# Performance work log

Hardware: AMD Instinct MI355X
Metric: run time of the kernel (lower is better)

## Reference

```python
import jax, jax.numpy as jnp
import numpy as np

INPUT_SIZE = 784
HIDDEN_SIZE = 256
NUM_CLASSES = 10
BATCH = 32768


def setup_inputs() -> dict:
    key = jax.random.key(0)
    k_x, k_w1, k_b1, k_w2, k_b2 = jax.random.split(key, 5)
    return {
        "x": jax.random.normal(k_x, (BATCH, INPUT_SIZE), dtype=jnp.float32),
        "fc1_weight": jax.random.normal(k_w1, (HIDDEN_SIZE, INPUT_SIZE), dtype=jnp.float32),
        "fc1_bias": jax.random.normal(k_b1, (HIDDEN_SIZE,), dtype=jnp.float32),
        "fc2_weight": jax.random.normal(k_w2, (NUM_CLASSES, HIDDEN_SIZE), dtype=jnp.float32),
        "fc2_bias": jax.random.normal(k_b2, (NUM_CLASSES,), dtype=jnp.float32),
    }


def reference(x, fc1_weight, fc1_bias, fc2_weight, fc2_bias):
    # hidden = x @ W1^T + b1, ReLU
    hidden = jnp.einsum("bi,hi->bh", x, fc1_weight) + fc1_bias
    activated = jnp.maximum(hidden, 0.0)
    # output = activated @ W2^T + b2
    logits = jnp.einsum("bh,ch->bc", activated, fc2_weight) + fc2_bias
    return jax.nn.softmax(logits, axis=-1)
```

## Files before the change

### kernel.cpp

```cpp
#include <hip/hip_runtime.h>
#include <math.h>

#define BATCH_N   32768
#define IN_F      784
#define HID_F     256
#define NCLS      10
#define BM        64
#define BK        32
#define NKT       25
#define NTHREADS  256

typedef __attribute__((ext_vector_type(8))) short short8;
typedef __attribute__((ext_vector_type(4))) float f32x4;

#define WS_W1H 0
#define WS_W1L 409600

union S8U { short8 s; uint4 u; };

__device__ __forceinline__ void cvt8(float4 a, float4 b, short8* hi, short8* lo) {
    const unsigned M = 0xFFFF0000u;
    const unsigned ux = __float_as_uint(a.x), uy = __float_as_uint(a.y),
                   uz = __float_as_uint(a.z), uw = __float_as_uint(a.w),
                   vx = __float_as_uint(b.x), vy = __float_as_uint(b.y),
                   vz = __float_as_uint(b.z), vw = __float_as_uint(b.w);
    S8U h, l;
    h.u.x = (ux >> 16) | (uy & M);
    h.u.y = (uz >> 16) | (uw & M);
    h.u.z = (vx >> 16) | (vy & M);
    h.u.w = (vz >> 16) | (vw & M);
    const float rx = a.x - __uint_as_float(ux & M);
    const float ry = a.y - __uint_as_float(uy & M);
    const float rz = a.z - __uint_as_float(uz & M);
    const float rw = a.w - __uint_as_float(uw & M);
    const float sx = b.x - __uint_as_float(vx & M);
    const float sy = b.y - __uint_as_float(vy & M);
    const float sz = b.z - __uint_as_float(vz & M);
    const float sw_ = b.w - __uint_as_float(vw & M);
    l.u.x = (__float_as_uint(rx) >> 16) | (__float_as_uint(ry) & M);
    l.u.y = (__float_as_uint(rz) >> 16) | (__float_as_uint(rw) & M);
    l.u.z = (__float_as_uint(sx) >> 16) | (__float_as_uint(sy) & M);
    l.u.w = (__float_as_uint(sz) >> 16) | (__float_as_uint(sw_) & M);
    *hi = h.s; *lo = l.s;
}

__global__ __launch_bounds__(256)
void prep_w1_kernel(const float* __restrict__ w1, char* __restrict__ ws) {
    const int s    = blockIdx.x * 256 + threadIdx.x;
    const int lane = s & 63, ct = (s >> 6) & 15, kt = s >> 10;
    const int n    = ct * 16 + (lane & 15);
    const int k0   = kt * 32 + (lane >> 4) * 8;
    float4 a = make_float4(0.f, 0.f, 0.f, 0.f), b = a;
    if (k0 + 7 < IN_F) {
        const float* p = w1 + (size_t)n * IN_F + k0;
        a = *(const float4*)p;
        b = *(const float4*)(p + 4);
    }
    short8 hi, lo;
    cvt8(a, b, &hi, &lo);
    *(short8*)(ws + WS_W1H + (size_t)s * 16) = hi;
    *(short8*)(ws + WS_W1L + (size_t)s * 16) = lo;
}

__global__ __launch_bounds__(NTHREADS, 2)
void mlp_mfma_kernel(const float* __restrict__ x,
                     const char*  __restrict__ wsb,
                     const float* __restrict__ b1,
                     const float* __restrict__ w2,
                     const float* __restrict__ b2,
                     float* __restrict__ out)
{
    __shared__ float hid[BM * HID_F];

    const int tid  = threadIdx.x;
    const int wv   = tid >> 6;
    const int lane = tid & 63;
    const int m    = lane & 15;
    const int quad = lane >> 4;
    const int row0 = blockIdx.x * BM;
    const int kq   = quad * 8;

    f32x4 acc[4][4];
    #pragma unroll
    for (int a = 0; a < 4; ++a)
        #pragma unroll
        for (int b = 0; b < 4; ++b)
            acc[a][b] = (f32x4){0.f, 0.f, 0.f, 0.f};

    const float* xb[4];
    #pragma unroll
    for (int rt = 0; rt < 4; ++rt)
        xb[rt] = x + (size_t)(row0 + rt * 16 + m) * IN_F;

    const char* bhp = wsb + WS_W1H + ((size_t)(wv * 4) * 64 + lane) * 16;
    const char* blp = wsb + WS_W1L + ((size_t)(wv * 4) * 64 + lane) * 16;

    float4 xc[4][2];
    short8 bhc[4], blc[4];
    #pragma unroll
    for (int rt = 0; rt < 4; ++rt) {
        xc[rt][0] = *(const float4*)(xb[rt] + kq);
        xc[rt][1] = *(const float4*)(xb[rt] + kq + 4);
    }
    #pragma unroll
    for (int c = 0; c < 4; ++c) {
        bhc[c] = *(const short8*)(bhp + c * 1024);
        blc[c] = *(const short8*)(blp + c * 1024);
    }

    #pragma unroll 8
    for (int kt = 0; kt < NKT - 1; ++kt) {
        short8 bhn[4], bln[4];
        #pragma unroll
        for (int c = 0; c < 4; ++c) {
            bhn[c] = *(const short8*)(bhp + (size_t)(kt + 1) * 16384 + c * 1024);
            bln[c] = *(const short8*)(blp + (size_t)(kt + 1) * 16384 + c * 1024);
        }
        int kon = (kt + 1) * BK + kq;
        kon = kon > (IN_F - 8) ? (IN_F - 8) : kon;
        float4 xn[4][2];
        #pragma unroll
        for (int rt = 0; rt < 4; ++rt) {
            xn[rt][0] = *(const float4*)(xb[rt] + kon);
            xn[rt][1] = *(const float4*)(xb[rt] + kon + 4);
        }
        short8 ah[4], al[4];
        #pragma unroll
        for (int rt = 0; rt < 4; ++rt)
            cvt8(xc[rt][0], xc[rt][1], &ah[rt], &al[rt]);
        #pragma unroll
        for (int rt = 0; rt < 4; ++rt)
            #pragma unroll
            for (int c = 0; c < 4; ++c) {
                acc[rt][c] = __builtin_amdgcn_mfma_f32_16x16x32_bf16(ah[rt], bhc[c], acc[rt][c], 0, 0, 0);
                acc[rt][c] = __builtin_amdgcn_mfma_f32_16x16x32_bf16(al[rt], bhc[c], acc[rt][c], 0, 0, 0);
                acc[rt][c] = __builtin_amdgcn_mfma_f32_16x16x32_bf16(ah[rt], blc[c], acc[rt][c], 0, 0, 0);
            }
        #pragma unroll
        for (int rt = 0; rt < 4; ++rt) {
            xc[rt][0] = xn[rt][0];
            xc[rt][1] = xn[rt][1];
        }
        #pragma unroll
        for (int c = 0; c < 4; ++c) { bhc[c] = bhn[c]; blc[c] = bln[c]; }
    }

    {
        short8 ah[4], al[4];
        #pragma unroll
        for (int rt = 0; rt < 4; ++rt)
            cvt8(xc[rt][0], xc[rt][1], &ah[rt], &al[rt]);
        if (quad >= 2) {
            const short8 zz = {0, 0, 0, 0, 0, 0, 0, 0};
            #pragma unroll
            for (int rt = 0; rt < 4; ++rt) { ah[rt] = zz; al[rt] = zz; }
        }
        #pragma unroll
        for (int rt = 0; rt < 4; ++rt)
            #pragma unroll
            for (int c = 0; c < 4; ++c) {
                acc[rt][c] = __builtin_amdgcn_mfma_f32_16x16x32_bf16(ah[rt], bhc[c], acc[rt][c], 0, 0, 0);
                acc[rt][c] = __builtin_amdgcn_mfma_f32_16x16x32_bf16(al[rt], bhc[c], acc[rt][c], 0, 0, 0);
                acc[rt][c] = __builtin_amdgcn_mfma_f32_16x16x32_bf16(ah[rt], blc[c], acc[rt][c], 0, 0, 0);
            }
    }

    #pragma unroll
    for (int c = 0; c < 4; ++c) {
        const int col = (wv * 4 + c) * 16 + m;
        const float bv = b1[col];
        #pragma unroll
        for (int rt = 0; rt < 4; ++rt)
            #pragma unroll
            for (int reg = 0; reg < 4; ++reg) {
                const int row = rt * 16 + quad * 4 + reg;
                hid[row * 256 + (col ^ ((row & 7) << 2))] = fmaxf(acc[rt][c][reg] + bv, 0.f);
            }
    }
    __syncthreads();

    const int rl = wv * 16 + m;
    const int sw = (rl & 7) << 2;
    const float* hrow = hid + rl * 256;
    float lg[NCLS];
    #pragma unroll
    for (int c = 0; c < NCLS; ++c) lg[c] = 0.f;
    #pragma unroll
    for (int i = 0; i < 8; ++i) {
        const int h0 = i * 32 + quad * 8;
        const float4 h1 = *(const float4*)(hrow + (h0 ^ sw));
        const float4 h2 = *(const float4*)(hrow + ((h0 + 4) ^ sw));
        #pragma unroll
        for (int c = 0; c < NCLS; ++c) {
            const float4 wa = *(const float4*)(w2 + c * HID_F + h0);
            const float4 wb = *(const float4*)(w2 + c * HID_F + h0 + 4);
            lg[c] += h1.x * wa.x + h1.y * wa.y + h1.z * wa.z + h1.w * wa.w
                   + h2.x * wb.x + h2.y * wb.y + h2.z * wb.z + h2.w * wb.w;
        }
    }
    #pragma unroll
    for (int c = 0; c < NCLS; ++c) {
        float v = lg[c];
        v += __shfl_xor(v, 16);
        v += __shfl_xor(v, 32);
        lg[c] = v;
    }
    if (quad == 0) {
        float mx = -1e30f;
        #pragma unroll
        for (int c = 0; c < NCLS; ++c) { lg[c] += b2[c]; mx = fmaxf(mx, lg[c]); }
        float s = 0.f;
        #pragma unroll
        for (int c = 0; c < NCLS; ++c) { lg[c] = __expf(lg[c] - mx); s += lg[c]; }
        const float inv = 1.f / s;
        float* o = out + (size_t)(row0 + rl) * NCLS;
        #pragma unroll
        for (int c = 0; c < NCLS; ++c) o[c] = lg[c] * inv;
    }
}

extern "C" void kernel_launch(void* const* d_in, const int* in_sizes, int n_in,
                              void* d_out, int out_size, void* d_ws, size_t ws_size,
                              hipStream_t stream)
{
    const float* x  = (const float*)d_in[0];
    const float* w1 = (const float*)d_in[1];
    const float* b1 = (const float*)d_in[2];
    const float* w2 = (const float*)d_in[3];
    const float* b2 = (const float*)d_in[4];
    float* out = (float*)d_out;

    hipLaunchKernelGGL(prep_w1_kernel, dim3(100), dim3(256), 0, stream,
                       w1, (char*)d_ws);
    hipLaunchKernelGGL(mlp_mfma_kernel, dim3(BATCH_N / BM), dim3(NTHREADS), 0, stream,
                       x, (const char*)d_ws, b1, w2, b2, out);
}
```

Baseline: 200.6 us.

## Stage split-bf16 X tiles in LDS with 512-thread blocks and double buffering

The GEMM1 mainloop now loads each X row segment once per block, converts it to bf16 hi/lo and stores it in double-buffered, XOR-swizzled LDS. Eight waves split the work as 2 row groups by 4 column groups, replacing per-wave redundant global X loads and repeated conversions. The hidden tile is written to shared memory in two halves to shrink LDS, and the epilogue is reworked so 8 threads per row each reduce a slice. In exchange the loop gains a __syncthreads per 64-wide k step, and the W1 fragments are no longer register-prefetched a step ahead.

```diff
diff --git a/kernel.cpp b/kernel.cpp
--- a/kernel.cpp
+++ b/kernel.cpp
@@ -6,9 +6,8 @@
 #define HID_F     256
 #define NCLS      10
 #define BM        64
-#define BK        32
-#define NKT       25
-#define NTHREADS  256
+#define NTHREADS  512
+#define NRND      13
 
 typedef __attribute__((ext_vector_type(8))) short short8;
 typedef __attribute__((ext_vector_type(4))) float f32x4;
@@ -62,7 +61,7 @@
     *(short8*)(ws + WS_W1L + (size_t)s * 16) = lo;
 }
 
-__global__ __launch_bounds__(NTHREADS, 2)
+__global__ __launch_bounds__(NTHREADS, 4)
 void mlp_mfma_kernel(const float* __restrict__ x,
                      const char*  __restrict__ wsb,
                      const float* __restrict__ b1,
@@ -70,153 +69,174 @@
                      const float* __restrict__ b2,
                      float* __restrict__ out)
 {
-    __shared__ float hid[BM * HID_F];
+    __shared__ short8 xh[2][512];
+    __shared__ short8 xl[2][512];
+    __shared__ float  hid[64 * 128];
 
     const int tid  = threadIdx.x;
+    const int lane = tid & 63;
     const int wv   = tid >> 6;
-    const int lane = tid & 63;
+    const int wc   = wv & 3;
+    const int wr   = wv >> 2;
     const int m    = lane & 15;
     const int quad = lane >> 4;
     const int row0 = blockIdx.x * BM;
-    const int kq   = quad * 8;
-
-    f32x4 acc[4][4];
-    #pragma unroll
-    for (int a = 0; a < 4; ++a)
+
+    const int slr = tid >> 3;
+    const int sks = tid & 7;
+    const float* xs = x + (size_t)(row0 + slr) * IN_F + sks * 8;
+    const int swidx = slr * 8 + (sks ^ (slr & 7));
+
+    const int rb  = (wr * 32 + m) * 8;
+    const int sl0 = rb + (quad ^ (m & 7));
+    const int sl1 = rb + ((4 + quad) ^ (m & 7));
+
+    const char* bhp = wsb + WS_W1H + ((size_t)(wc * 4) * 64 + lane) * 16;
+    const char* blp = wsb + WS_W1L + ((size_t)(wc * 4) * 64 + lane) * 16;
+
+    f32x4 acc[2][4];
+    #pragma unroll
+    for (int a = 0; a < 2; ++a)
         #pragma unroll
         for (int b = 0; b < 4; ++b)
             acc[a][b] = (f32x4){0.f, 0.f, 0.f, 0.f};
 
-    const float* xb[4];
-    #pragma unroll
-    for (int rt = 0; rt < 4; ++rt)
-        xb[rt] = x + (size_t)(row0 + rt * 16 + m) * IN_F;
-
-    const char* bhp = wsb + WS_W1H + ((size_t)(wv * 4) * 64 + lane) * 16;
-    const char* blp = wsb + WS_W1L + ((size_t)(wv * 4) * 64 + lane) * 16;
-
-    float4 xc[4][2];
-    short8 bhc[4], blc[4];
-    #pragma unroll
-    for (int rt = 0; rt < 4; ++rt) {
-        xc[rt][0] = *(const float4*)(xb[rt] + kq);
-        xc[rt][1] = *(const float4*)(xb[rt] + kq + 4);
-    }
-    #pragma unroll
-    for (int c = 0; c < 4; ++c) {
-        bhc[c] = *(const short8*)(bhp + c * 1024);
-        blc[c] = *(const short8*)(blp + c * 1024);
-    }
-
-    #pragma unroll 8
-    for (int kt = 0; kt < NKT - 1; ++kt) {
-        short8 bhn[4], bln[4];
+    {
+        float4 a = *(const float4*)(xs);
+        float4 b = *(const float4*)(xs + 4);
+        short8 hi, lo;
+        cvt8(a, b, &hi, &lo);
+        xh[0][swidx] = hi;
+        xl[0][swidx] = lo;
+    }
+    __syncthreads();
+
+    int cur = 0;
+    for (int r = 0; r < NRND - 1; ++r) {
+        const int kn = (r + 1) * 64 + sks * 8;
+        float4 xa = make_float4(0.f, 0.f, 0.f, 0.f), xb = xa;
+        if (kn + 7 < IN_F) {
+            xa = *(const float4*)(xs + (r + 1) * 64);
+            xb = *(const float4*)(xs + (r + 1) * 64 + 4);
+        }
+        #pragma unroll
+        for (int kk = 0; kk < 2; ++kk) {
+            const int kt = r * 2 + kk;
+            short8 bh[4], bl[4];
+            #pragma unroll
+            for (int c = 0; c < 4; ++c) {
+                bh[c] = *(const short8*)(bhp + (size_t)kt * 16384 + c * 1024);
+                bl[c] = *(const short8*)(blp + (size_t)kt * 16384 + c * 1024);
+            }
+            const int sl = kk ? sl1 : sl0;
+            short8 ah[2], al[2];
+            #pragma unroll
+            for (int rt = 0; rt < 2; ++rt) {
+                ah[rt] = xh[cur][sl + rt * 128];
+                al[rt] = xl[cur][sl + rt * 128];
+            }
+            #pragma unroll
+            for (int rt = 0; rt < 2; ++rt)
+                #pragma unroll
+                for (int c = 0; c < 4; ++c) {
+                    acc[rt][c] = __builtin_amdgcn_mfma_f32_16x16x32_bf16(ah[rt], bh[c], acc[rt][c], 0, 0, 0);
+                    acc[rt][c] = __builtin_amdgcn_mfma_f32_16x16x32_bf16(al[rt], bh[c], acc[rt][c], 0, 0, 0);
+                    acc[rt][c] = __builtin_amdgcn_mfma_f32_16x16x32_bf16(ah[rt], bl[c], acc[rt][c], 0, 0, 0);
+                }
+        }
+        {
+            short8 hi, lo;
+            cvt8(xa, xb, &hi, &lo);
+            xh[cur ^ 1][swidx] = hi;
+            xl[cur ^ 1][swidx] = lo;
+        }
+        __syncthreads();
+        cur ^= 1;
+    }
+
+    {
+        const int kt = 24;
+        short8 bh[4], bl[4];
         #pragma unroll
         for (int c = 0; c < 4; ++c) {
-            bhn[c] = *(const short8*)(bhp + (size_t)(kt + 1) * 16384 + c * 1024);
-            bln[c] = *(const short8*)(blp + (size_t)(kt + 1) * 16384 + c * 1024);
-        }
-        int kon = (kt + 1) * BK + kq;
-        kon = kon > (IN_F - 8) ? (IN_F - 8) : kon;
-        float4 xn[4][2];
-        #pragma unroll
-        for (int rt = 0; rt < 4; ++rt) {
-            xn[rt][0] = *(const float4*)(xb[rt] + kon);
-            xn[rt][1] = *(const float4*)(xb[rt] + kon + 4);
-        }
-        short8 ah[4], al[4];
-        #pragma unroll
-        for (int rt = 0; rt < 4; ++rt)
-            cvt8(xc[rt][0], xc[rt][1], &ah[rt], &al[rt]);
-        #pragma unroll
-        for (int rt = 0; rt < 4; ++rt)
+            bh[c] = *(const short8*)(bhp + (size_t)kt * 16384 + c * 1024);
+            bl[c] = *(const short8*)(blp + (size_t)kt * 16384 + c * 1024);
+        }
+        short8 ah[2], al[2];
+        #pragma unroll
+        for (int rt = 0; rt < 2; ++rt) {
+            ah[rt] = xh[cur][sl0 + rt * 128];
+            al[rt] = xl[cur][sl0 + rt * 128];
+        }
+        #pragma unroll
+        for (int rt = 0; rt < 2; ++rt)
             #pragma unroll
             for (int c = 0; c < 4; ++c) {
-                acc[rt][c] = __builtin_amdgcn_mfma_f32_16x16x32_bf16(ah[rt], bhc[c], acc[rt][c], 0, 0, 0);
-                acc[rt][c] = __builtin_amdgcn_mfma_f32_16x16x32_bf16(al[rt], bhc[c], acc[rt][c], 0, 0, 0);
-                acc[rt][c] = __builtin_amdgcn_mfma_f32_16x16x32_bf16(ah[rt], blc[c], acc[rt][c], 0, 0, 0);
-            }
-        #pragma unroll
-        for (int rt = 0; rt < 4; ++rt) {
-            xc[rt][0] = xn[rt][0];
-            xc[rt][1] = xn[rt][1];
-        }
-        #pragma unroll
-        for (int c = 0; c < 4; ++c) { bhc[c] = bhn[c]; blc[c] = bln[c]; }
-    }
-
-    {
-        short8 ah[4], al[4];
-        #pragma unroll
-        for (int rt = 0; rt < 4; ++rt)
-            cvt8(xc[rt][0], xc[rt][1], &ah[rt], &al[rt]);
-        if (quad >= 2) {
-            const short8 zz = {0, 0, 0, 0, 0, 0, 0, 0};
-            #pragma unroll
-            for (int rt = 0; rt < 4; ++rt) { ah[rt] = zz; al[rt] = zz; }
-        }
-        #pragma unroll
-        for (int rt = 0; rt < 4; ++rt)
-            #pragma unroll
-            for (int c = 0; c < 4; ++c) {
-                acc[rt][c] = __builtin_amdgcn_mfma_f32_16x16x32_bf16(ah[rt], bhc[c], acc[rt][c], 0, 0, 0);
-                acc[rt][c] = __builtin_amdgcn_mfma_f32_16x16x32_bf16(al[rt], bhc[c], acc[rt][c], 0, 0, 0);
-                acc[rt][c] = __builtin_amdgcn_mfma_f32_16x16x32_bf16(ah[rt], blc[c], acc[rt][c], 0, 0, 0);
-            }
-    }
-
-    #pragma unroll
-    for (int c = 0; c < 4; ++c) {
-        const int col = (wv * 4 + c) * 16 + m;
-        const float bv = b1[col];
-        #pragma unroll
-        for (int rt = 0; rt < 4; ++rt)
-            #pragma unroll
-            for (int reg = 0; reg < 4; ++reg) {
-                const int row = rt * 16 + quad * 4 + reg;
-                hid[row * 256 + (col ^ ((row & 7) << 2))] = fmaxf(acc[rt][c][reg] + bv, 0.f);
-            }
-    }
-    __syncthreads();
-
-    const int rl = wv * 16 + m;
-    const int sw = (rl & 7) << 2;
-    const float* hrow = hid + rl * 256;
+                acc[rt][c] = __builtin_amdgcn_mfma_f32_16x16x32_bf16(ah[rt], bh[c], acc[rt][c], 0, 0, 0);
+                acc[rt][c] = __builtin_amdgcn_mfma_f32_16x16x32_bf16(al[rt], bh[c], acc[rt][c], 0, 0, 0);
+                acc[rt][c] = __builtin_amdgcn_mfma_f32_16x16x32_bf16(ah[rt], bl[c], acc[rt][c], 0, 0, 0);
+            }
+    }
+
+    const int rl    = tid >> 3;
+    const int slice = tid & 7;
+    const int gb    = (slice >> 1) * 64 + (slice & 1) * 16;
+    const int cb    = slice * 16;
+    const int sw2   = (rl & 7) << 2;
+
     float lg[NCLS];
     #pragma unroll
-    for (int c = 0; c < NCLS; ++c) lg[c] = 0.f;
-    #pragma unroll
-    for (int i = 0; i < 8; ++i) {
-        const int h0 = i * 32 + quad * 8;
-        const float4 h1 = *(const float4*)(hrow + (h0 ^ sw));
-        const float4 h2 = *(const float4*)(hrow + ((h0 + 4) ^ sw));
-        #pragma unroll
-        for (int c = 0; c < NCLS; ++c) {
-            const float4 wa = *(const float4*)(w2 + c * HID_F + h0);
-            const float4 wb = *(const float4*)(w2 + c * HID_F + h0 + 4);
-            lg[c] += h1.x * wa.x + h1.y * wa.y + h1.z * wa.z + h1.w * wa.w
-                   + h2.x * wb.x + h2.y * wb.y + h2.z * wb.z + h2.w * wb.w;
-        }
-    }
-    #pragma unroll
-    for (int c = 0; c < NCLS; ++c) {
-        float v = lg[c];
-        v += __shfl_xor(v, 16);
-        v += __shfl_xor(v, 32);
-        lg[c] = v;
-    }
-    if (quad == 0) {
-        float mx = -1e30f;
-        #pragma unroll
-        for (int c = 0; c < NCLS; ++c) { lg[c] += b2[c]; mx = fmaxf(mx, lg[c]); }
-        float s = 0.f;
-        #pragma unroll
-        for (int c = 0; c < NCLS; ++c) { lg[c] = __expf(lg[c] - mx); s += lg[c]; }
-        const float inv = 1.f / s;
-        float* o = out + (size_t)(row0 + rl) * NCLS;
-        #pragma unroll
-        for (int c = 0; c < NCLS; ++c) o[c] = lg[c] * inv;
-    }
+    for (int k = 0; k < NCLS; ++k) lg[k] = 0.f;
+
+    #pragma unroll
+    for (int p = 0; p < 2; ++p) {
+        __syncthreads();
+        #pragma unroll
+        for (int cl = 0; cl < 2; ++cl) {
+            const int c  = 2 * p + cl;
+            const int g  = (wc * 4 + c) * 16 + m;
+            const float bv = b1[g];
+            const int cc = wc * 32 + cl * 16 + m;
+            #pragma unroll
+            for (int rt = 0; rt < 2; ++rt)
+                #pragma unroll
+                for (int reg = 0; reg < 4; ++reg) {
+                    const int row = wr * 32 + rt * 16 + quad * 4 + reg;
+                    hid[row * 128 + (cc ^ ((row & 7) << 2))] =
+                        fmaxf(acc[rt][c][reg] + bv, 0.f);
+                }
+        }
+        __syncthreads();
+        #pragma unroll
+        for (int i = 0; i < 4; ++i) {
+            const float4 h = *(const float4*)(hid + rl * 128 + ((cb + i * 4) ^ sw2));
+            const int g4 = gb + 32 * p + i * 4;
+            #pragma unroll
+            for (int k = 0; k < NCLS; ++k) {
+                const float4 w = *(const float4*)(w2 + k * HID_F + g4);
+                lg[k] += h.x * w.x + h.y * w.y + h.z * w.z + h.w * w.w;
+            }
+        }
+    }
+
+    #pragma unroll
+    for (int k = 0; k < NCLS; ++k) {
+        float v = lg[k];
+        v += __shfl_xor(v, 1);
+        v += __shfl_xor(v, 2);
+        v += __shfl_xor(v, 4);
+        lg[k] = v + b2[k];
+    }
+    float mx = -1e30f;
+    #pragma unroll
+    for (int k = 0; k < NCLS; ++k) mx = fmaxf(mx, lg[k]);
+    float s = 0.f;
+    #pragma unroll
+    for (int k = 0; k < NCLS; ++k) { lg[k] = __expf(lg[k] - mx); s += lg[k]; }
+    const float inv = 1.f / s;
+    float* o = out + (size_t)(row0 + rl) * NCLS;
+    o[slice] = lg[slice] * inv;
+    if (slice < 2) o[8 + slice] = lg[8 + slice] * inv;
 }
 
 extern "C" void kernel_launch(void* const* d_in, const int* in_sizes, int n_in,
```

New measurement: 206.2 us. 1.03x slower.
